# Performance work log

Measured on AMD Instinct MI355X. Metric: run time of the kernel, lower is better.

The kernel has to match this reference:

```python
import jax, jax.numpy as jnp
import numpy as np

ALPHA = 2.0
EROSIONS = 10
# 2D cross structuring element * 0.2, same as cv.getStructuringElement(cv.MORPH_CROSS,(3,3))*0.2
KERNEL2D = jnp.array([[0.0, 0.2, 0.0],
                      [0.2, 0.2, 0.2],
                      [0.0, 0.2, 0.0]], dtype=jnp.float32)


def setup_inputs() -> dict:
    key = jax.random.key(0)
    k1, k2 = jax.random.split(key)
    B, C, H, W = 8, 8, 512, 512
    x = jax.random.uniform(k1, (B, C, H, W), dtype=jnp.float32)
    y = jax.random.uniform(k2, (B, C, H, W), dtype=jnp.float32)
    return {"x": x, "y": y}


def reference(x, y):
    # bound = (pred - target)^2, shape (B, C, H, W)
    bound = (x - y) ** 2
    B, C, H, W = bound.shape
    # batch all (b, cls) images into one conv: (B*C, 1, H, W)
    cur = bound.reshape(B * C, 1, H, W)
    kern = KERNEL2D.reshape(1, 1, 3, 3)  # OIHW; kernel is symmetric so conv == correlate

    def step(carry, k):
        cur, acc = carry
        # scipy convolve(mode='constant', cval=0) == SAME zero-padded conv
        dil = jax.lax.conv_general_dilated(cur, kern, window_strides=(1, 1),
                                           padding='SAME',
                                           dimension_numbers=('NCHW', 'OIHW', 'NCHW'))
        ero = jnp.maximum(dil - 0.5, 0.0)
        # per-image global min-max normalization iff ptp != 0
        mn = ero.min(axis=(1, 2, 3), keepdims=True)
        mx = ero.max(axis=(1, 2, 3), keepdims=True)
        ptp = mx - mn
        normed = (ero - mn) / jnp.where(ptp > 0, ptp, 1.0)
        ero = jnp.where(ptp > 0, normed, ero)
        acc = acc + ero * (k.astype(ero.dtype) + 1.0) ** ALPHA
        return (ero, acc), None

    (_, eroted), _ = jax.lax.scan(step, (cur, jnp.zeros_like(cur)),
                                  jnp.arange(EROSIONS))
    # batch_dice=False -> plain mean over everything
    return eroted.mean()
```

## Files before the change

### kernel.cpp

```cpp
#include <hip/hip_runtime.h>

#define IMGS 64
#define HH 512
#define WW 512
#define NPIX (HH * WW)
#define STEPS 10
#define RSTRIP 8
#define TILE_ROWS 16
#define BLKS_PER_IMG 32
#define NBLK (IMGS * BLKS_PER_IMG)
#define WPI 128

template <int FIRST>
__global__ __launch_bounds__(256) void kconv(const float* __restrict__ xg,
                                             const float* __restrict__ yg,
                                             const float* __restrict__ src,
                                             float* __restrict__ dst,
                                             const float* __restrict__ pMin,
                                             const float* __restrict__ pMax,
                                             float2* __restrict__ pmm,
                                             double* __restrict__ psum) {
    const int bid = blockIdx.x;
    const int swz = (bid & 7) * (NBLK / 8) + (bid >> 3);
    const int img = swz >> 5;
    const int blk = swz & 31;
    const int tid = threadIdx.x;
    const int w = tid >> 6;
    const int lane = tid & 63;
    const int h = w & 1;
    const int g = w >> 1;
    const int vc = h * 64 + lane;
    const int ys = blk * TILE_ROWS + g * RSTRIP;
    const size_t base = (size_t)img * NPIX;

    float scale = 1.0f, off = 0.0f;
    if (!FIRST) {
        float mn = pMin[img];
        float ptp = pMax[img] - mn;
        if (ptp > 0.0f) { scale = 1.0f / ptp; off = mn * scale; }
    }

    const float4* xv = (const float4*)(xg + base);
    const float4* yv = (const float4*)(yg + base);
    const float4* sv = (const float4*)(src + base);

    auto ld4 = [&](int r) -> float4 {
        if (FIRST) {
            float4 a = xv[r * 128 + vc];
            float4 b = yv[r * 128 + vc];
            float4 v;
            v.x = (a.x - b.x) * (a.x - b.x);
            v.y = (a.y - b.y) * (a.y - b.y);
            v.z = (a.z - b.z) * (a.z - b.z);
            v.w = (a.w - b.w) * (a.w - b.w);
            return v;
        } else {
            float4 v = sv[r * 128 + vc];
            v.x = fmaf(v.x, scale, -off);
            v.y = fmaf(v.y, scale, -off);
            v.z = fmaf(v.z, scale, -off);
            v.w = fmaf(v.w, scale, -off);
            return v;
        }
    };
    auto ld1 = [&](int r, int pcol) -> float {
        if (FIRST) {
            float d = xg[base + r * WW + pcol] - yg[base + r * WW + pcol];
            return d * d;
        } else {
            return fmaf(src[base + r * WW + pcol], scale, -off);
        }
    };

    const float4 z4 = make_float4(0.f, 0.f, 0.f, 0.f);
    float4 pm1 = (ys > 0) ? ld4(ys - 1) : z4;
    float4 p0 = ld4(ys);

    float tmin = __uint_as_float(0x7f800000u);
    float tmax = 0.0f;
    float tsum = 0.0f;
    float4* dv = (float4*)(dst + base);

    #pragma unroll
    for (int i = 0; i < RSTRIP; ++i) {
        const int y = ys + i;
        float4 p1 = (y + 1 < HH) ? ld4(y + 1) : z4;

        float lf = __shfl_up(p0.w, 1);
        float rt = __shfl_down(p0.x, 1);
        if (lane == 0)  lf = (vc > 0)   ? ld1(y, vc * 4 - 1) : 0.0f;
        if (lane == 63) rt = (vc < 127) ? ld1(y, vc * 4 + 4) : 0.0f;

        float4 e;
        e.x = 0.2f * (pm1.x + p1.x + lf   + p0.x + p0.y);
        e.y = 0.2f * (pm1.y + p1.y + p0.x + p0.y + p0.z);
        e.z = 0.2f * (pm1.z + p1.z + p0.y + p0.z + p0.w);
        e.w = 0.2f * (pm1.w + p1.w + p0.z + p0.w + rt);
        e.x = fmaxf(e.x - 0.5f, 0.0f);
        e.y = fmaxf(e.y - 0.5f, 0.0f);
        e.z = fmaxf(e.z - 0.5f, 0.0f);
        e.w = fmaxf(e.w - 0.5f, 0.0f);

        dv[y * 128 + vc] = e;

        tmin = fminf(tmin, fminf(fminf(e.x, e.y), fminf(e.z, e.w)));
        tmax = fmaxf(tmax, fmaxf(fmaxf(e.x, e.y), fmaxf(e.z, e.w)));
        tsum += (e.x + e.y) + (e.z + e.w);

        pm1 = p0;
        p0 = p1;
    }

    double dsum = (double)tsum;
    #pragma unroll
    for (int o2 = 32; o2 > 0; o2 >>= 1) {
        tmin = fminf(tmin, __shfl_down(tmin, o2));
        tmax = fmaxf(tmax, __shfl_down(tmax, o2));
        dsum += __shfl_down(dsum, o2);
    }

    if (lane == 0) {
        const int idx = img * WPI + blk * 4 + w;
        pmm[idx] = make_float2(tmin, tmax);
        psum[idx] = dsum;
    }
}

__global__ __launch_bounds__(128) void kred(const float2* __restrict__ pmm,
                                            const double* __restrict__ psum,
                                            float* __restrict__ oMin,
                                            float* __restrict__ oMax,
                                            double* __restrict__ oSum) {
    const int img = blockIdx.x;
    const int tid = threadIdx.x;
    const int w = tid >> 6;
    const int lane = tid & 63;

    float2 mm = pmm[img * WPI + tid];
    double s = psum[img * WPI + tid];
    float tmin = mm.x, tmax = mm.y;

    #pragma unroll
    for (int o2 = 32; o2 > 0; o2 >>= 1) {
        tmin = fminf(tmin, __shfl_down(tmin, o2));
        tmax = fmaxf(tmax, __shfl_down(tmax, o2));
        s += __shfl_down(s, o2);
    }
    __shared__ float smin[2], smax[2];
    __shared__ double ssum[2];
    if (lane == 0) { smin[w] = tmin; smax[w] = tmax; ssum[w] = s; }
    __syncthreads();
    if (tid == 0) {
        oMin[img] = fminf(smin[0], smin[1]);
        oMax[img] = fmaxf(smax[0], smax[1]);
        oSum[img] = ssum[0] + ssum[1];
    }
}

__global__ void kfinal(const float* __restrict__ accMin,
                       const float* __restrict__ accMax,
                       const double* __restrict__ accSum,
                       float* __restrict__ out) {
    const int i = threadIdx.x;
    double tot = 0.0;
    for (int k = 0; k < STEPS; ++k) {
        float mn = accMin[k * IMGS + i];
        float ptp = accMax[k * IMGS + i] - mn;
        double S = accSum[k * IMGS + i];
        double sn = (ptp > 0.0f)
                        ? (S - (double)NPIX * (double)mn) / (double)ptp
                        : S;
        tot += sn * (double)((k + 1) * (k + 1));
    }
    #pragma unroll
    for (int o2 = 32; o2 > 0; o2 >>= 1) tot += __shfl_down(tot, o2);
    if (i == 0) out[0] = (float)(tot / ((double)IMGS * (double)NPIX));
}

extern "C" void kernel_launch(void* const* d_in, const int* in_sizes, int n_in,
                              void* d_out, int out_size, void* d_ws, size_t ws_size,
                              hipStream_t stream) {
    const float* x = (const float*)d_in[0];
    const float* y = (const float*)d_in[1];
    float* out = (float*)d_out;

    char* ws = (char*)d_ws;
    const size_t bufBytes = (size_t)IMGS * NPIX * sizeof(float);
    float* bufA = (float*)ws;
    float* bufB = (float*)(ws + bufBytes);
    char* p = ws + 2 * bufBytes;
    float2* pmm = (float2*)p;                 p += IMGS * WPI * sizeof(float2);
    double* psum = (double*)p;                p += IMGS * WPI * sizeof(double);
    float* accMin = (float*)p;                p += STEPS * IMGS * sizeof(float);
    float* accMax = (float*)p;                p += STEPS * IMGS * sizeof(float);
    double* accSum = (double*)p;

    kconv<1><<<NBLK, 256, 0, stream>>>(x, y, nullptr, bufA,
                                       nullptr, nullptr, pmm, psum);
    kred<<<IMGS, 128, 0, stream>>>(pmm, psum, accMin, accMax, accSum);

    float* cur = bufA;
    float* nxt = bufB;
    for (int k = 1; k < STEPS; ++k) {
        kconv<0><<<NBLK, 256, 0, stream>>>(
            nullptr, nullptr, cur, nxt,
            accMin + (k - 1) * IMGS, accMax + (k - 1) * IMGS, pmm, psum);
        kred<<<IMGS, 128, 0, stream>>>(pmm, psum, accMin + k * IMGS,
                                       accMax + k * IMGS, accSum + k * IMGS);
        float* tmp = cur; cur = nxt; nxt = tmp;
    }

    kfinal<<<1, 64, 0, stream>>>(accMin, accMax, accSum, out);
}
```

Before: 269.8 us.

## Fold per-image reductions into conv kernels and skip final buffer store

Removes the separate per-step reduction kernel: each conv kernel now reduces the previous step's per-wave min/max partials itself, and all per-step partials are kept so the final kernels compute the normalized sums. The last erosion step no longer writes its output image, since only its statistics are used. This cuts nine kernel launches and one full-image store, at the cost of every block redundantly reading 128 partials and running a wave reduction.

New measurement: 251.6 us. 6.7% less time.

```diff
diff --git a/kernel.cpp b/kernel.cpp
--- a/kernel.cpp
+++ b/kernel.cpp
@@ -11,13 +11,12 @@
 #define NBLK (IMGS * BLKS_PER_IMG)
 #define WPI 128
 
-template <int FIRST>
+template <int FIRST, int STORE>
 __global__ __launch_bounds__(256) void kconv(const float* __restrict__ xg,
                                              const float* __restrict__ yg,
                                              const float* __restrict__ src,
                                              float* __restrict__ dst,
-                                             const float* __restrict__ pMin,
-                                             const float* __restrict__ pMax,
+                                             const float2* __restrict__ prevMM,
                                              float2* __restrict__ pmm,
                                              double* __restrict__ psum) {
     const int bid = blockIdx.x;
@@ -35,9 +34,17 @@
 
     float scale = 1.0f, off = 0.0f;
     if (!FIRST) {
-        float mn = pMin[img];
-        float ptp = pMax[img] - mn;
-        if (ptp > 0.0f) { scale = 1.0f / ptp; off = mn * scale; }
+        float2 a = prevMM[img * WPI + lane];
+        float2 b = prevMM[img * WPI + 64 + lane];
+        float tmn = fminf(a.x, b.x);
+        float tmx = fmaxf(a.y, b.y);
+        #pragma unroll
+        for (int o2 = 32; o2 > 0; o2 >>= 1) {
+            tmn = fminf(tmn, __shfl_xor(tmn, o2));
+            tmx = fmaxf(tmx, __shfl_xor(tmx, o2));
+        }
+        float ptp = tmx - tmn;
+        if (ptp > 0.0f) { scale = 1.0f / ptp; off = tmn * scale; }
     }
 
     const float4* xv = (const float4*)(xg + base);
@@ -101,7 +108,7 @@
         e.z = fmaxf(e.z - 0.5f, 0.0f);
         e.w = fmaxf(e.w - 0.5f, 0.0f);
 
-        dv[y * 128 + vc] = e;
+        if (STORE) dv[y * 128 + vc] = e;
 
         tmin = fminf(tmin, fminf(fminf(e.x, e.y), fminf(e.z, e.w)));
         tmax = fmaxf(tmax, fmaxf(fmaxf(e.x, e.y), fmaxf(e.z, e.w)));
@@ -126,55 +133,41 @@
     }
 }
 
-__global__ __launch_bounds__(128) void kred(const float2* __restrict__ pmm,
+__global__ __launch_bounds__(64) void kfin1(const float2* __restrict__ pmm,
                                             const double* __restrict__ psum,
-                                            float* __restrict__ oMin,
-                                            float* __restrict__ oMax,
-                                            double* __restrict__ oSum) {
+                                            double* __restrict__ perImg) {
     const int img = blockIdx.x;
-    const int tid = threadIdx.x;
-    const int w = tid >> 6;
-    const int lane = tid & 63;
-
-    float2 mm = pmm[img * WPI + tid];
-    double s = psum[img * WPI + tid];
-    float tmin = mm.x, tmax = mm.y;
-
-    #pragma unroll
-    for (int o2 = 32; o2 > 0; o2 >>= 1) {
-        tmin = fminf(tmin, __shfl_down(tmin, o2));
-        tmax = fmaxf(tmax, __shfl_down(tmax, o2));
-        s += __shfl_down(s, o2);
-    }
-    __shared__ float smin[2], smax[2];
-    __shared__ double ssum[2];
-    if (lane == 0) { smin[w] = tmin; smax[w] = tmax; ssum[w] = s; }
-    __syncthreads();
-    if (tid == 0) {
-        oMin[img] = fminf(smin[0], smin[1]);
-        oMax[img] = fmaxf(smax[0], smax[1]);
-        oSum[img] = ssum[0] + ssum[1];
-    }
-}
-
-__global__ void kfinal(const float* __restrict__ accMin,
-                       const float* __restrict__ accMax,
-                       const double* __restrict__ accSum,
-                       float* __restrict__ out) {
-    const int i = threadIdx.x;
+    const int lane = threadIdx.x;
     double tot = 0.0;
     for (int k = 0; k < STEPS; ++k) {
-        float mn = accMin[k * IMGS + i];
-        float ptp = accMax[k * IMGS + i] - mn;
-        double S = accSum[k * IMGS + i];
+        const int o = (k * IMGS + img) * WPI;
+        float2 a = pmm[o + lane];
+        float2 b = pmm[o + 64 + lane];
+        double s = psum[o + lane] + psum[o + 64 + lane];
+        float tmn = fminf(a.x, b.x);
+        float tmx = fmaxf(a.y, b.y);
+        #pragma unroll
+        for (int o2 = 32; o2 > 0; o2 >>= 1) {
+            tmn = fminf(tmn, __shfl_xor(tmn, o2));
+            tmx = fmaxf(tmx, __shfl_xor(tmx, o2));
+            s += __shfl_xor(s, o2);
+        }
+        float ptp = tmx - tmn;
         double sn = (ptp > 0.0f)
-                        ? (S - (double)NPIX * (double)mn) / (double)ptp
-                        : S;
+                        ? (s - (double)NPIX * (double)tmn) / (double)ptp
+                        : s;
         tot += sn * (double)((k + 1) * (k + 1));
     }
+    if (lane == 0) perImg[img] = tot;
+}
+
+__global__ void kfin2(const double* __restrict__ perImg,
+                      float* __restrict__ out) {
+    double v = perImg[threadIdx.x];
     #pragma unroll
-    for (int o2 = 32; o2 > 0; o2 >>= 1) tot += __shfl_down(tot, o2);
-    if (i == 0) out[0] = (float)(tot / ((double)IMGS * (double)NPIX));
+    for (int o2 = 32; o2 > 0; o2 >>= 1) v += __shfl_down(v, o2);
+    if (threadIdx.x == 0)
+        out[0] = (float)(v / ((double)IMGS * (double)NPIX));
 }
 
 extern "C" void kernel_launch(void* const* d_in, const int* in_sizes, int n_in,
@@ -189,26 +182,28 @@
     float* bufA = (float*)ws;
     float* bufB = (float*)(ws + bufBytes);
     char* p = ws + 2 * bufBytes;
-    float2* pmm = (float2*)p;                 p += IMGS * WPI * sizeof(float2);
-    double* psum = (double*)p;                p += IMGS * WPI * sizeof(double);
-    float* accMin = (float*)p;                p += STEPS * IMGS * sizeof(float);
-    float* accMax = (float*)p;                p += STEPS * IMGS * sizeof(float);
-    double* accSum = (double*)p;
-
-    kconv<1><<<NBLK, 256, 0, stream>>>(x, y, nullptr, bufA,
-                                       nullptr, nullptr, pmm, psum);
-    kred<<<IMGS, 128, 0, stream>>>(pmm, psum, accMin, accMax, accSum);
-
+    float2* pmm = (float2*)p;        p += (size_t)STEPS * IMGS * WPI * sizeof(float2);
+    double* psum = (double*)p;       p += (size_t)STEPS * IMGS * WPI * sizeof(double);
+    double* perImg = (double*)p;
+
+    kconv<1, 1><<<NBLK, 256, 0, stream>>>(x, y, nullptr, bufA, nullptr,
+                                          pmm, psum);
     float* cur = bufA;
     float* nxt = bufB;
-    for (int k = 1; k < STEPS; ++k) {
-        kconv<0><<<NBLK, 256, 0, stream>>>(
+    for (int k = 1; k < STEPS - 1; ++k) {
+        kconv<0, 1><<<NBLK, 256, 0, stream>>>(
             nullptr, nullptr, cur, nxt,
-            accMin + (k - 1) * IMGS, accMax + (k - 1) * IMGS, pmm, psum);
-        kred<<<IMGS, 128, 0, stream>>>(pmm, psum, accMin + k * IMGS,
-                                       accMax + k * IMGS, accSum + k * IMGS);
+            pmm + (size_t)(k - 1) * IMGS * WPI,
+            pmm + (size_t)k * IMGS * WPI,
+            psum + (size_t)k * IMGS * WPI);
         float* tmp = cur; cur = nxt; nxt = tmp;
     }
-
-    kfinal<<<1, 64, 0, stream>>>(accMin, accMax, accSum, out);
-}
+    kconv<0, 0><<<NBLK, 256, 0, stream>>>(
+        nullptr, nullptr, cur, nullptr,
+        pmm + (size_t)(STEPS - 2) * IMGS * WPI,
+        pmm + (size_t)(STEPS - 1) * IMGS * WPI,
+        psum + (size_t)(STEPS - 1) * IMGS * WPI);
+
+    kfin1<<<IMGS, 64, 0, stream>>>(pmm, psum, perImg);
+    kfin2<<<1, 64, 0, stream>>>(perImg, out);
+}
```
